# Kernel optimization log

Hardware: AMD Instinct MI355X
Metric: run time of the kernel (lower is better)

The kernel has to match this reference:

```python
import jax, jax.numpy as jnp
import numpy as np

N_NODES = 50000
N_EDGES = 800000
IN_C, HID_C, OUT_C = 128, 128, 64
BN_EPS = 1e-5


def _normalized_adj(edge_index, N):
    # Mirrors remove_self_loops + add_self_loops + symmetric GCN normalization.
    src, dst = edge_index[0], edge_index[1]
    mask = (src != dst).astype(jnp.float32)  # drop original self loops
    # degree of dst over (masked edges + added self loops)
    deg = jax.ops.segment_sum(mask, dst, num_segments=N) + 1.0
    dinv = jnp.where(deg > 0, deg ** -0.5, 0.0)
    w = mask * dinv[src] * dinv[dst]          # weights for original edges
    w_self = dinv * dinv                      # weights for added self loops
    return src, dst, w, w_self


def _spmm(src, dst, w, w_self, x):
    # torch.sparse.mm(adj, x): out[i] = sum_{e: src[e]=i} w[e] * x[dst[e]] + w_self[i]*x[i]
    agg = jax.ops.segment_sum(w[:, None] * x[dst], src, num_segments=x.shape[0])
    return agg + w_self[:, None] * x


def setup_inputs() -> dict:
    key = jax.random.key(0)
    ks = jax.random.split(key, 4)
    x = jax.random.normal(ks[0], (N_NODES, IN_C), dtype=jnp.float32)
    edge_index = jax.random.randint(ks[1], (2, N_EDGES), 0, N_NODES, dtype=jnp.int64)
    # glorot init for GCN linear weights
    s1 = np.sqrt(6.0 / (IN_C + HID_C)).astype(np.float32)
    s2 = np.sqrt(6.0 / (HID_C + OUT_C)).astype(np.float32)
    W1 = jax.random.uniform(ks[2], (IN_C, HID_C), jnp.float32, -s1, s1)
    W2 = jax.random.uniform(ks[3], (HID_C, OUT_C), jnp.float32, -s2, s2)
    return {
        "x": x,
        "edge_index": edge_index,
        "W1": W1,
        "b1": jnp.zeros((HID_C,), jnp.float32),
        "gamma": jnp.ones((HID_C,), jnp.float32),
        "beta": jnp.zeros((HID_C,), jnp.float32),
        "W2": W2,
        "b2": jnp.zeros((OUT_C,), jnp.float32),
    }


def reference(x, edge_index, W1, b1, gamma, beta, W2, b2):
    N = x.shape[0]
    src, dst, w, w_self = _normalized_adj(edge_index, N)
    # layer 1: linear -> SpMM -> BN (batch stats) -> ReLU (dropout: eval)
    h = x @ W1 + b1
    h = _spmm(src, dst, w, w_self, h)
    mean = h.mean(axis=0)
    var = jnp.mean((h - mean) ** 2, axis=0)
    h = (h - mean) * jax.lax.rsqrt(var + BN_EPS) * gamma + beta
    h = jax.nn.relu(h)
    # layer 2: linear -> SpMM
    h = h @ W2 + b2
    h = _spmm(src, dst, w, w_self, h)
    return h
```

## Files before the change

kernel.cpp:

```cpp
#include <hip/hip_runtime.h>

#define N_NODES 50000
#define N_EDGES 800000
#define BN_EPS 1e-5f
#define NPAD 50176
#define SCAN_BLOCKS 98

#define S_SLICES 64
#define R_RANGES 4
#define BINS 16384
#define NP4 (R_RANGES * BINS)
#define ES (N_EDGES / S_SLICES)

#define XS_STRIDE 68

typedef unsigned int uint;
typedef unsigned short ushort;
typedef float floatx4 __attribute__((ext_vector_type(4)));
typedef short bf16x8 __attribute__((ext_vector_type(8)));

__device__ __forceinline__ float bfl(uint u) { return __uint_as_float(u << 16); }
__device__ __forceinline__ float bfh(uint u) { return __uint_as_float(u & 0xffff0000u); }
__device__ __forceinline__ uint pack_bf2(float a, float b) {
    uint ua = __float_as_uint(a), ub = __float_as_uint(b);
    ua += 0x7fffu + ((ua >> 16) & 1u);
    ub += 0x7fffu + ((ub >> 16) & 1u);
    return (ua >> 16) | (ub & 0xffff0000u);
}
__device__ __forceinline__ ushort bf1(float x) {
    uint u = __float_as_uint(x);
    u += 0x7fffu + ((u >> 16) & 1u);
    return (ushort)(u >> 16);
}
__device__ __forceinline__ void acc8(float* a, uint4 h, float w) {
    a[0] += w * bfl(h.x); a[1] += w * bfh(h.x);
    a[2] += w * bfl(h.y); a[3] += w * bfh(h.y);
    a[4] += w * bfl(h.z); a[5] += w * bfh(h.z);
    a[6] += w * bfl(h.w); a[7] += w * bfh(h.w);
}

__global__ __launch_bounds__(256) void prep_w_kernel(const float* __restrict__ W1,
                                                     const float* __restrict__ W2,
                                                     uint* __restrict__ W1t,
                                                     uint* __restrict__ W2t) {
    int t = blockIdx.x * 256 + threadIdx.x;
    if (t < 8192) {
        int n = t >> 6, kk = t & 63;
        W1t[t] = pack_bf2(W1[(2 * kk) * 128 + n], W1[(2 * kk + 1) * 128 + n]);
    } else if (t < 12288) {
        int u = t - 8192;
        int n = u >> 6, kk = u & 63;
        W2t[u] = pack_bf2(W2[(2 * kk) * 64 + n], W2[(2 * kk + 1) * 64 + n]);
    }
}

__global__ __launch_bounds__(256) void count_hist_kernel(const int* __restrict__ src,
                                                         const int* __restrict__ dst,
                                                         ushort* __restrict__ part_cnt,
                                                         ushort* __restrict__ part_deg) {
    __shared__ uint cnt_lds[BINS / 2];
    __shared__ uint deg_lds[BINS / 2];
    const int s = blockIdx.x / R_RANGES;
    const int r = blockIdx.x % R_RANGES;
    const int base = r * BINS;
    for (int j = threadIdx.x; j < BINS / 2; j += 256) { cnt_lds[j] = 0u; deg_lds[j] = 0u; }
    __syncthreads();
    const int4* s4 = (const int4*)(src + s * ES);
    const int4* d4 = (const int4*)(dst + s * ES);
#pragma unroll 2
    for (int g = threadIdx.x; g < ES / 4; g += 256) {
        int4 sv = s4[g];
        int4 dv = d4[g];
#pragma unroll
        for (int k = 0; k < 4; ++k) {
            int ss = (&sv.x)[k], dd = (&dv.x)[k];
            if (ss != dd) {
                int a = ss - base;
                if ((unsigned)a < (unsigned)BINS)
                    atomicAdd(&cnt_lds[a >> 1], 1u << ((a & 1) * 16));
                int b = dd - base;
                if ((unsigned)b < (unsigned)BINS)
                    atomicAdd(&deg_lds[b >> 1], 1u << ((b & 1) * 16));
            }
        }
    }
    __syncthreads();
    uint* pc = (uint*)&part_cnt[s * NP4 + base];
    uint* pd = (uint*)&part_deg[s * NP4 + base];
    for (int j = threadIdx.x; j < BINS / 2; j += 256) { pc[j] = cnt_lds[j]; pd[j] = deg_lds[j]; }
}

__global__ __launch_bounds__(256) void reduce_scan_kernel(const ushort* __restrict__ part_deg,
                                                          const ushort* __restrict__ part_cnt,
                                                          float* __restrict__ dinv,
                                                          int* __restrict__ rowcnt,
                                                          int* __restrict__ rowptr,
                                                          int* __restrict__ psum,
                                                          float* __restrict__ stats) {
    const int t = threadIdx.x;
    if (blockIdx.x == 0) stats[t] = 0.f;
    const int i = blockIdx.x * 512 + 2 * t;
    uint dg0 = 0, dg1 = 0, rc0 = 0, rc1 = 0;
#pragma unroll 8
    for (int s = 0; s < S_SLICES; ++s) {
        uint vd = *(const uint*)&part_deg[s * NP4 + i];
        uint vc = *(const uint*)&part_cnt[s * NP4 + i];
        dg0 += vd & 0xffffu; dg1 += vd >> 16;
        rc0 += vc & 0xffffu; rc1 += vc >> 16;
    }
    *(int2*)&rowcnt[i] = make_int2((int)rc0, (int)rc1);
    if (i < N_NODES) dinv[i] = rsqrtf((float)dg0 + 1.0f);
    if (i + 1 < N_NODES) dinv[i + 1] = rsqrtf((float)dg1 + 1.0f);

    __shared__ int bs[256];
    const int pair = (int)(rc0 + rc1);
    bs[t] = pair;
    __syncthreads();
#pragma unroll
    for (int off = 1; off < 256; off <<= 1) {
        int x = (t >= off) ? bs[t - off] : 0;
        __syncthreads();
        bs[t] += x;
        __syncthreads();
    }
    const int excl = bs[t] - pair;
    *(int2*)&rowptr[i] = make_int2(excl + (int)rc0, excl + pair);
    if (t == 255) psum[blockIdx.x] = bs[255];
}

__global__ __launch_bounds__(256) void cursor_init_kernel(const int* __restrict__ rowcnt,
                                                          int* __restrict__ rowptr,
                                                          const int* __restrict__ psum,
                                                          const ushort* __restrict__ part_cnt,
                                                          int* __restrict__ cursor) {
    __shared__ int pbuf[SCAN_BLOCKS];
    __shared__ int lps;
    const int t = threadIdx.x;
    if (t < SCAN_BLOCKS) pbuf[t] = psum[t];
    __syncthreads();
    if (t == 0) {
        int acc = 0;
        for (int j = 0; j < (int)blockIdx.x; ++j) acc += pbuf[j];
        lps = acc;
    }
    __syncthreads();
    const int ps = lps;
    const int i = blockIdx.x * 512 + 2 * t;
    int b0 = rowptr[i] - rowcnt[i] + ps;
    int b1 = rowptr[i + 1] - rowcnt[i + 1] + ps;
    *(int2*)&rowptr[i] = make_int2(b0, b1);
#pragma unroll 8
    for (int s = 0; s < S_SLICES; ++s) {
        *(int2*)&cursor[s * NP4 + i] = make_int2(b0, b1);
        uint vc = *(const uint*)&part_cnt[s * NP4 + i];
        b0 += (int)(vc & 0xffffu);
        b1 += (int)(vc >> 16);
    }
}

__global__ __launch_bounds__(256) void fill_lds_kernel(const int* __restrict__ src,
                                                       const int* __restrict__ dst,
                                                       const float* __restrict__ dinv,
                                                       const int* __restrict__ cursor,
                                                       int2* __restrict__ epair) {
    __shared__ int curs[BINS];
    const int s = blockIdx.x / R_RANGES;
    const int r = blockIdx.x % R_RANGES;
    const int base = r * BINS;
    const int* gc = &cursor[s * NP4 + base];
    for (int j = threadIdx.x; j < BINS; j += 256) curs[j] = gc[j];
    __syncthreads();
    const int4* s4 = (const int4*)(src + s * ES);
    const int4* d4 = (const int4*)(dst + s * ES);
#pragma unroll 2
    for (int g = threadIdx.x; g < ES / 4; g += 256) {
        int4 sv = s4[g];
        int4 dv = d4[g];
#pragma unroll
        for (int k = 0; k < 4; ++k) {
            int ss = (&sv.x)[k], dd = (&dv.x)[k];
            int a = ss - base;
            if (ss != dd && (unsigned)a < (unsigned)BINS) {
                int pos = atomicAdd(&curs[a], 1);
                epair[pos] = make_int2(dd, __float_as_int(dinv[ss] * dinv[dd]));
            }
        }
    }
}

__global__ __launch_bounds__(256) void gemm1_mfma_kernel(const float* __restrict__ X,
                                                         const uint* __restrict__ W1t,
                                                         const float* __restrict__ bias,
                                                         ushort* __restrict__ Hbf) {
    __shared__ uint lds[(64 + 128) * XS_STRIDE];
    uint* Xs = lds;
    uint* Ws = lds + 64 * XS_STRIDE;
    const int t = threadIdx.x;
    const int rowBase = blockIdx.x * 64;

    {
        int r = t >> 2, q = t & 3;
        int arow = rowBase + r;
        uint* xd = &Xs[r * XS_STRIDE + q * 16];
        if (arow < N_NODES) {
            const float4* xp = (const float4*)&X[arow * 128 + q * 32];
#pragma unroll
            for (int i = 0; i < 8; ++i) {
                float4 v = xp[i];
                xd[2 * i]     = pack_bf2(v.x, v.y);
                xd[2 * i + 1] = pack_bf2(v.z, v.w);
            }
        } else {
#pragma unroll
            for (int i = 0; i < 16; ++i) xd[i] = 0u;
        }
    }
    {
        int n = t >> 1, half = t & 1;
        const uint4* wp = (const uint4*)&W1t[n * 64 + half * 32];
        uint* wd = &Ws[n * XS_STRIDE + half * 32];
#pragma unroll
        for (int i = 0; i < 8; ++i) *(uint4*)&wd[i * 4] = wp[i];
    }
    __syncthreads();

    const int wv = t >> 6, lane = t & 63;
    const int lr = lane & 15;
    const int ko = (lane >> 4) * 4;
    const int m0 = wv * 16;
    floatx4 acc[8];
#pragma unroll
    for (int j = 0; j < 8; ++j) acc[j] = (floatx4){0.f, 0.f, 0.f, 0.f};

#pragma unroll
    for (int ks = 0; ks < 4; ++ks) {
        const int kb = ks * 16 + ko;
        bf16x8 a = *(bf16x8*)&Xs[(m0 + lr) * XS_STRIDE + kb];
#pragma unroll
        for (int j = 0; j < 8; ++j) {
            bf16x8 b = *(bf16x8*)&Ws[(j * 16 + lr) * XS_STRIDE + kb];
            acc[j] = __builtin_amdgcn_mfma_f32_16x16x32_bf16(a, b, acc[j], 0, 0, 0);
        }
    }
    const int rbase = rowBase + m0 + (lane >> 4) * 4;
#pragma unroll
    for (int j = 0; j < 8; ++j) {
        const int col = j * 16 + lr;
        const float bb = bias[col];
#pragma unroll
        for (int r = 0; r < 4; ++r) {
            int row = rbase + r;
            if (row < N_NODES) Hbf[row * 128 + col] = bf1(acc[j][r] + bb);
        }
    }
}

__global__ __launch_bounds__(256) void gemm2_mfma_kernel(const uint* __restrict__ Hin,
                                                         const uint* __restrict__ W2t,
                                                         const float* __restrict__ bias,
                                                         const float* __restrict__ sum,
                                                         const float* __restrict__ sumsq,
                                                         const float* __restrict__ gamma,
                                                         const float* __restrict__ beta,
                                                         ushort* __restrict__ Hbf) {
    __shared__ uint lds[(64 + 64) * XS_STRIDE];
    __shared__ float sc_sh[128], sh_sh[128];
    uint* Xs = lds;
    uint* Ws = lds + 64 * XS_STRIDE;
    const int t = threadIdx.x;
    const int rowBase = blockIdx.x * 64;

    if (t < 128) {
        float mean = sum[t] * (1.0f / N_NODES);
        float var = sumsq[t] * (1.0f / N_NODES) - mean * mean;
        float sc = gamma[t] * rsqrtf(var + BN_EPS);
        sc_sh[t] = sc;
        sh_sh[t] = beta[t] - mean * sc;
    }
    if (t >= 128) {
        int u = t - 128;
        int n = u >> 1, half = u & 1;
        const uint4* wp = (const uint4*)&W2t[n * 64 + half * 32];
        uint* wd = &Ws[n * XS_STRIDE + half * 32];
#pragma unroll
        for (int i = 0; i < 8; ++i) *(uint4*)&wd[i * 4] = wp[i];
    }
    __syncthreads();

    {
        int r = t >> 2, q = t & 3;
        int arow = rowBase + r;
        uint* xd = &Xs[r * XS_STRIDE + q * 16];
        if (arow < N_NODES) {
            const uint* hp = &Hin[arow * 64 + q * 16];
#pragma unroll
            for (int i = 0; i < 16; ++i) {
                uint u = hp[i];
                int m = q * 16 + i;
                float a0 = fmaxf(0.f, bfl(u) * sc_sh[2 * m] + sh_sh[2 * m]);
                float a1 = fmaxf(0.f, bfh(u) * sc_sh[2 * m + 1] + sh_sh[2 * m + 1]);
                xd[i] = pack_bf2(a0, a1);
            }
        } else {
#pragma unroll
            for (int i = 0; i < 16; ++i) xd[i] = 0u;
        }
    }
    __syncthreads();

    const int wv = t >> 6, lane = t & 63;
    const int lr = lane & 15;
    const int ko = (lane >> 4) * 4;
    const int m0 = wv * 16;
    floatx4 acc[4];
#pragma unroll
    for (int j = 0; j < 4; ++j) acc[j] = (floatx4){0.f, 0.f, 0.f, 0.f};

#pragma unroll
    for (int ks = 0; ks < 4; ++ks) {
        const int kb = ks * 16 + ko;
        bf16x8 a = *(bf16x8*)&Xs[(m0 + lr) * XS_STRIDE + kb];
#pragma unroll
        for (int j = 0; j < 4; ++j) {
            bf16x8 b = *(bf16x8*)&Ws[(j * 16 + lr) * XS_STRIDE + kb];
            acc[j] = __builtin_amdgcn_mfma_f32_16x16x32_bf16(a, b, acc[j], 0, 0, 0);
        }
    }
    const int rbase = rowBase + m0 + (lane >> 4) * 4;
#pragma unroll
    for (int j = 0; j < 4; ++j) {
        const int col = j * 16 + lr;
        const float bb = bias[col];
#pragma unroll
        for (int r = 0; r < 4; ++r) {
            int row = rbase + r;
            if (row < N_NODES) Hbf[row * 64 + col] = bf1(acc[j][r] + bb);
        }
    }
}

template <int C, bool OUT_BF16>
__global__ __launch_bounds__(256) void spmm_bf16_kernel(const int* __restrict__ rowptr,
                                                        const int2* __restrict__ epair,
                                                        const float* __restrict__ dinv,
                                                        const uint* __restrict__ H,
                                                        void* __restrict__ outv) {
    constexpr int LPR = C / 8;
    constexpr int RPB = 256 / LPR;
    constexpr int US  = C / 2;
    const int t = threadIdx.x;
    const int lane = t % LPR;
    const int row = blockIdx.x * RPB + t / LPR;
    if (row >= N_NODES) return;
    const int cu = lane * 4;
    const float di = dinv[row];

    float acc[8];
    {
        uint4 hv = *(const uint4*)&H[row * US + cu];
        float w = di * di;
        acc[0] = w * bfl(hv.x); acc[1] = w * bfh(hv.x);
        acc[2] = w * bfl(hv.y); acc[3] = w * bfh(hv.y);
        acc[4] = w * bfl(hv.z); acc[5] = w * bfh(hv.z);
        acc[6] = w * bfl(hv.w); acc[7] = w * bfh(hv.w);
    }
    const int e0 = rowptr[row], e1 = rowptr[row + 1];
    int e = e0;
    if ((e & 1) && e < e1) {
        int2 p = epair[e];
        uint4 h = *(const uint4*)&H[p.x * US + cu];
        acc8(acc, h, __int_as_float(p.y));
        ++e;
    }
    const int4* ep4 = (const int4*)epair;
    for (; e + 8 <= e1; e += 8) {
        int4 qa = ep4[(e >> 1) + 0];
        int4 qb = ep4[(e >> 1) + 1];
        int4 qc = ep4[(e >> 1) + 2];
        int4 qd = ep4[(e >> 1) + 3];
        uint4 h0 = *(const uint4*)&H[qa.x * US + cu];
        uint4 h1 = *(const uint4*)&H[qa.z * US + cu];
        uint4 h2 = *(const uint4*)&H[qb.x * US + cu];
        uint4 h3 = *(const uint4*)&H[qb.z * US + cu];
        uint4 h4 = *(const uint4*)&H[qc.x * US + cu];
        uint4 h5 = *(const uint4*)&H[qc.z * US + cu];
        uint4 h6 = *(const uint4*)&H[qd.x * US + cu];
        uint4 h7 = *(const uint4*)&H[qd.z * US + cu];
        acc8(acc, h0, __int_as_float(qa.y));
        acc8(acc, h1, __int_as_float(qa.w));
        acc8(acc, h2, __int_as_float(qb.y));
        acc8(acc, h3, __int_as_float(qb.w));
        acc8(acc, h4, __int_as_float(qc.y));
        acc8(acc, h5, __int_as_float(qc.w));
        acc8(acc, h6, __int_as_float(qd.y));
        acc8(acc, h7, __int_as_float(qd.w));
    }
    for (; e + 2 <= e1; e += 2) {
        int4 q = ep4[e >> 1];
        uint4 h0 = *(const uint4*)&H[q.x * US + cu];
        uint4 h1 = *(const uint4*)&H[q.z * US + cu];
        acc8(acc, h0, __int_as_float(q.y));
        acc8(acc, h1, __int_as_float(q.w));
    }
    if (e < e1) {
        int2 p = epair[e];
        uint4 h = *(const uint4*)&H[p.x * US + cu];
        acc8(acc, h, __int_as_float(p.y));
    }
    if (OUT_BF16) {
        uint4 o;
        o.x = pack_bf2(acc[0], acc[1]);
        o.y = pack_bf2(acc[2], acc[3]);
        o.z = pack_bf2(acc[4], acc[5]);
        o.w = pack_bf2(acc[6], acc[7]);
        *(uint4*)&((uint*)outv)[row * US + cu] = o;
    } else {
        float* out = (float*)outv;
        *(float4*)&out[row * C + lane * 8]     = make_float4(acc[0], acc[1], acc[2], acc[3]);
        *(float4*)&out[row * C + lane * 8 + 4] = make_float4(acc[4], acc[5], acc[6], acc[7]);
    }
}

__global__ __launch_bounds__(256) void bn_stats_kernel(const uint* __restrict__ H,
                                                       float* __restrict__ sum,
                                                       float* __restrict__ sumsq) {
    int uc = threadIdx.x & 63;
    int quarter = threadIdx.x >> 6;
    float s0 = 0.f, q0 = 0.f, s1 = 0.f, q1 = 0.f;
    for (int r = blockIdx.x * 4 + quarter; r < N_NODES; r += 512) {
        uint u = H[r * 64 + uc];
        float a = bfl(u), b = bfh(u);
        s0 += a; q0 += a * a;
        s1 += b; q1 += b * b;
    }
    __shared__ float red[4][256];
    red[0][threadIdx.x] = s0; red[1][threadIdx.x] = q0;
    red[2][threadIdx.x] = s1; red[3][threadIdx.x] = q1;
    __syncthreads();
    if (quarter == 0) {
        float ts0 = 0.f, tq0 = 0.f, ts1 = 0.f, tq1 = 0.f;
#pragma unroll
        for (int k = 0; k < 4; ++k) {
            ts0 += red[0][k * 64 + uc]; tq0 += red[1][k * 64 + uc];
            ts1 += red[2][k * 64 + uc]; tq1 += red[3][k * 64 + uc];
        }
        atomicAdd(&sum[2 * uc], ts0);
        atomicAdd(&sum[2 * uc + 1], ts1);
        atomicAdd(&sumsq[2 * uc], tq0);
        atomicAdd(&sumsq[2 * uc + 1], tq1);
    }
}

extern "C" void kernel_launch(void* const* d_in, const int* in_sizes, int n_in,
                              void* d_out, int out_size, void* d_ws, size_t ws_size,
                              hipStream_t stream) {
    const float* x     = (const float*)d_in[0];
    const int*   ei    = (const int*)d_in[1];
    const float* W1    = (const float*)d_in[2];
    const float* b1    = (const float*)d_in[3];
    const float* gamma = (const float*)d_in[4];
    const float* beta  = (const float*)d_in[5];
    const float* W2    = (const float*)d_in[6];
    const float* b2    = (const float*)d_in[7];
    float* out = (float*)d_out;
    const int* src = ei;
    const int* dst = ei + N_EDGES;

    float* ws     = (float*)d_ws;
    float* dinv   = ws;
    float* stats  = ws + NPAD;
    int*   psum   = (int*)(ws + NPAD + 512);
    int*   rowcnt = psum + 128;
    int*   rowptr = rowcnt + NPAD;
    float* big    = (float*)(rowptr + NPAD);
    int2*   epair    = (int2*)big;
    ushort* part_cnt = (ushort*)(big + 1600000);
    ushort* part_deg = (ushort*)(big + 3700000);
    int*    cursor   = (int*)(big + 5800000);
    ushort* h1bf     = (ushort*)(big + 1600000);
    uint*   h1agg    = (uint*)(big + 4800000);
    ushort* h2bf     = h1bf;
    uint*   W1t      = (uint*)(big + 10000000);
    uint*   W2t      = W1t + 8192;
    float* sum    = stats;
    float* sumsq  = stats + 128;

    prep_w_kernel<<<48, 256, 0, stream>>>(W1, W2, W1t, W2t);

    count_hist_kernel<<<S_SLICES * R_RANGES, 256, 0, stream>>>(src, dst, part_cnt, part_deg);
    reduce_scan_kernel<<<SCAN_BLOCKS, 256, 0, stream>>>(part_deg, part_cnt, dinv, rowcnt,
                                                        rowptr, psum, stats);
    cursor_init_kernel<<<SCAN_BLOCKS, 256, 0, stream>>>(rowcnt, rowptr, psum, part_cnt, cursor);
    fill_lds_kernel<<<S_SLICES * R_RANGES, 256, 0, stream>>>(src, dst, dinv, cursor, epair);

    gemm1_mfma_kernel<<<(N_NODES + 63) / 64, 256, 0, stream>>>(x, W1t, b1, h1bf);

    spmm_bf16_kernel<128, true><<<(N_NODES + 15) / 16, 256, 0, stream>>>(
        rowptr, epair, dinv, (const uint*)h1bf, (void*)h1agg);

    bn_stats_kernel<<<128, 256, 0, stream>>>(h1agg, sum, sumsq);

    gemm2_mfma_kernel<<<(N_NODES + 63) / 64, 256, 0, stream>>>(h1agg, W2t, b2, sum, sumsq,
                                                               gamma, beta, h2bf);

    spmm_bf16_kernel<64, false><<<(N_NODES + 31) / 32, 256, 0, stream>>>(
        rowptr, epair, dinv, (const uint*)h2bf, (void*)out);
}
```

Measured before the change: 244.9 us.

## Fuse BN statistics into SpMM, merge weight prep into histogram, use byte counters

The batch-norm sum and sum-of-squares are now accumulated inside the first SpMM through LDS atomics, followed by one global atomic per channel per block. This removes the separate bn_stats pass that re-read the aggregated layer-1 output. Weight transposition and packing moves into an extra block of the histogram kernel, saving a launch. Per-slice histogram counters shrink from 16 to 8 bits, halving partial-count traffic, but a node that gets 256 or more edges in one slice would overflow its counter. The statistics are also taken from fp32 accumulators before bf16 rounding rather than from the stored bf16 values.

```diff
diff --git a/kernel.cpp b/kernel.cpp
--- a/kernel.cpp
+++ b/kernel.cpp
@@ -16,6 +16,7 @@
 
 typedef unsigned int uint;
 typedef unsigned short ushort;
+typedef unsigned char uchar;
 typedef float floatx4 __attribute__((ext_vector_type(4)));
 typedef short bf16x8 __attribute__((ext_vector_type(8)));
 
@@ -39,31 +40,33 @@
     a[6] += w * bfl(h.w); a[7] += w * bfh(h.w);
 }
 
-__global__ __launch_bounds__(256) void prep_w_kernel(const float* __restrict__ W1,
-                                                     const float* __restrict__ W2,
-                                                     uint* __restrict__ W1t,
-                                                     uint* __restrict__ W2t) {
-    int t = blockIdx.x * 256 + threadIdx.x;
-    if (t < 8192) {
-        int n = t >> 6, kk = t & 63;
-        W1t[t] = pack_bf2(W1[(2 * kk) * 128 + n], W1[(2 * kk + 1) * 128 + n]);
-    } else if (t < 12288) {
-        int u = t - 8192;
-        int n = u >> 6, kk = u & 63;
-        W2t[u] = pack_bf2(W2[(2 * kk) * 64 + n], W2[(2 * kk + 1) * 64 + n]);
-    }
-}
-
 __global__ __launch_bounds__(256) void count_hist_kernel(const int* __restrict__ src,
                                                          const int* __restrict__ dst,
-                                                         ushort* __restrict__ part_cnt,
-                                                         ushort* __restrict__ part_deg) {
-    __shared__ uint cnt_lds[BINS / 2];
-    __shared__ uint deg_lds[BINS / 2];
+                                                         const float* __restrict__ W1,
+                                                         const float* __restrict__ W2,
+                                                         uint* __restrict__ W1t,
+                                                         uint* __restrict__ W2t,
+                                                         uchar* __restrict__ part_cnt,
+                                                         uchar* __restrict__ part_deg) {
+    if (blockIdx.x == S_SLICES * R_RANGES) {
+        for (int t = threadIdx.x; t < 12288; t += 256) {
+            if (t < 8192) {
+                int n = t >> 6, kk = t & 63;
+                W1t[t] = pack_bf2(W1[(2 * kk) * 128 + n], W1[(2 * kk + 1) * 128 + n]);
+            } else {
+                int u = t - 8192;
+                int n = u >> 6, kk = u & 63;
+                W2t[u] = pack_bf2(W2[(2 * kk) * 64 + n], W2[(2 * kk + 1) * 64 + n]);
+            }
+        }
+        return;
+    }
+    __shared__ uint cnt_lds[BINS / 4];
+    __shared__ uint deg_lds[BINS / 4];
     const int s = blockIdx.x / R_RANGES;
     const int r = blockIdx.x % R_RANGES;
     const int base = r * BINS;
-    for (int j = threadIdx.x; j < BINS / 2; j += 256) { cnt_lds[j] = 0u; deg_lds[j] = 0u; }
+    for (int j = threadIdx.x; j < BINS / 4; j += 256) { cnt_lds[j] = 0u; deg_lds[j] = 0u; }
     __syncthreads();
     const int4* s4 = (const int4*)(src + s * ES);
     const int4* d4 = (const int4*)(dst + s * ES);
@@ -77,21 +80,21 @@
             if (ss != dd) {
                 int a = ss - base;
                 if ((unsigned)a < (unsigned)BINS)
-                    atomicAdd(&cnt_lds[a >> 1], 1u << ((a & 1) * 16));
+                    atomicAdd(&cnt_lds[a >> 2], 1u << ((a & 3) * 8));
                 int b = dd - base;
                 if ((unsigned)b < (unsigned)BINS)
-                    atomicAdd(&deg_lds[b >> 1], 1u << ((b & 1) * 16));
+                    atomicAdd(&deg_lds[b >> 2], 1u << ((b & 3) * 8));
             }
         }
     }
     __syncthreads();
     uint* pc = (uint*)&part_cnt[s * NP4 + base];
     uint* pd = (uint*)&part_deg[s * NP4 + base];
-    for (int j = threadIdx.x; j < BINS / 2; j += 256) { pc[j] = cnt_lds[j]; pd[j] = deg_lds[j]; }
-}
-
-__global__ __launch_bounds__(256) void reduce_scan_kernel(const ushort* __restrict__ part_deg,
-                                                          const ushort* __restrict__ part_cnt,
+    for (int j = threadIdx.x; j < BINS / 4; j += 256) { pc[j] = cnt_lds[j]; pd[j] = deg_lds[j]; }
+}
+
+__global__ __launch_bounds__(256) void reduce_scan_kernel(const uchar* __restrict__ part_deg,
+                                                          const uchar* __restrict__ part_cnt,
                                                           float* __restrict__ dinv,
                                                           int* __restrict__ rowcnt,
                                                           int* __restrict__ rowptr,
@@ -103,10 +106,10 @@
     uint dg0 = 0, dg1 = 0, rc0 = 0, rc1 = 0;
 #pragma unroll 8
     for (int s = 0; s < S_SLICES; ++s) {
-        uint vd = *(const uint*)&part_deg[s * NP4 + i];
-        uint vc = *(const uint*)&part_cnt[s * NP4 + i];
-        dg0 += vd & 0xffffu; dg1 += vd >> 16;
-        rc0 += vc & 0xffffu; rc1 += vc >> 16;
+        uint vd = *(const ushort*)&part_deg[s * NP4 + i];
+        uint vc = *(const ushort*)&part_cnt[s * NP4 + i];
+        dg0 += vd & 0xffu; dg1 += vd >> 8;
+        rc0 += vc & 0xffu; rc1 += vc >> 8;
     }
     *(int2*)&rowcnt[i] = make_int2((int)rc0, (int)rc1);
     if (i < N_NODES) dinv[i] = rsqrtf((float)dg0 + 1.0f);
@@ -131,7 +134,7 @@
 __global__ __launch_bounds__(256) void cursor_init_kernel(const int* __restrict__ rowcnt,
                                                           int* __restrict__ rowptr,
                                                           const int* __restrict__ psum,
-                                                          const ushort* __restrict__ part_cnt,
+                                                          const uchar* __restrict__ part_cnt,
                                                           int* __restrict__ cursor) {
     __shared__ int pbuf[SCAN_BLOCKS];
     __shared__ int lps;
@@ -152,9 +155,9 @@
 #pragma unroll 8
     for (int s = 0; s < S_SLICES; ++s) {
         *(int2*)&cursor[s * NP4 + i] = make_int2(b0, b1);
-        uint vc = *(const uint*)&part_cnt[s * NP4 + i];
-        b0 += (int)(vc & 0xffffu);
-        b1 += (int)(vc >> 16);
+        uint vc = *(const ushort*)&part_cnt[s * NP4 + i];
+        b0 += (int)(vc & 0xffu);
+        b1 += (int)(vc >> 8);
     }
 }
 
@@ -339,19 +342,25 @@
     }
 }
 
-template <int C, bool OUT_BF16>
+template <int C, bool OUT_BF16, bool BN>
 __global__ __launch_bounds__(256) void spmm_bf16_kernel(const int* __restrict__ rowptr,
                                                         const int2* __restrict__ epair,
                                                         const float* __restrict__ dinv,
                                                         const uint* __restrict__ H,
-                                                        void* __restrict__ outv) {
+                                                        void* __restrict__ outv,
+                                                        float* __restrict__ stats) {
     constexpr int LPR = C / 8;
     constexpr int RPB = 256 / LPR;
     constexpr int US  = C / 2;
+    __shared__ float bns[BN ? 256 : 1];
     const int t = threadIdx.x;
+    if (BN) {
+        bns[t] = 0.f;
+        __syncthreads();
+    }
     const int lane = t % LPR;
     const int row = blockIdx.x * RPB + t / LPR;
-    if (row >= N_NODES) return;
+    if (!BN && row >= N_NODES) return;
     const int cu = lane * 4;
     const float di = dinv[row];
 
@@ -419,35 +428,14 @@
         *(float4*)&out[row * C + lane * 8]     = make_float4(acc[0], acc[1], acc[2], acc[3]);
         *(float4*)&out[row * C + lane * 8 + 4] = make_float4(acc[4], acc[5], acc[6], acc[7]);
     }
-}
-
-__global__ __launch_bounds__(256) void bn_stats_kernel(const uint* __restrict__ H,
-                                                       float* __restrict__ sum,
-                                                       float* __restrict__ sumsq) {
-    int uc = threadIdx.x & 63;
-    int quarter = threadIdx.x >> 6;
-    float s0 = 0.f, q0 = 0.f, s1 = 0.f, q1 = 0.f;
-    for (int r = blockIdx.x * 4 + quarter; r < N_NODES; r += 512) {
-        uint u = H[r * 64 + uc];
-        float a = bfl(u), b = bfh(u);
-        s0 += a; q0 += a * a;
-        s1 += b; q1 += b * b;
-    }
-    __shared__ float red[4][256];
-    red[0][threadIdx.x] = s0; red[1][threadIdx.x] = q0;
-    red[2][threadIdx.x] = s1; red[3][threadIdx.x] = q1;
-    __syncthreads();
-    if (quarter == 0) {
-        float ts0 = 0.f, tq0 = 0.f, ts1 = 0.f, tq1 = 0.f;
-#pragma unroll
-        for (int k = 0; k < 4; ++k) {
-            ts0 += red[0][k * 64 + uc]; tq0 += red[1][k * 64 + uc];
-            ts1 += red[2][k * 64 + uc]; tq1 += red[3][k * 64 + uc];
-        }
-        atomicAdd(&sum[2 * uc], ts0);
-        atomicAdd(&sum[2 * uc + 1], ts1);
-        atomicAdd(&sumsq[2 * uc], tq0);
-        atomicAdd(&sumsq[2 * uc + 1], tq1);
+    if (BN) {
+#pragma unroll
+        for (int j = 0; j < 8; ++j) {
+            atomicAdd(&bns[lane * 8 + j], acc[j]);
+            atomicAdd(&bns[128 + lane * 8 + j], acc[j] * acc[j]);
+        }
+        __syncthreads();
+        atomicAdd(&stats[t], bns[t]);
     }
 }
 
@@ -474,8 +462,8 @@
     int*   rowptr = rowcnt + NPAD;
     float* big    = (float*)(rowptr + NPAD);
     int2*   epair    = (int2*)big;
-    ushort* part_cnt = (ushort*)(big + 1600000);
-    ushort* part_deg = (ushort*)(big + 3700000);
+    uchar*  part_cnt = (uchar*)(big + 1600000);
+    uchar*  part_deg = (uchar*)(big + 3700000);
     int*    cursor   = (int*)(big + 5800000);
     ushort* h1bf     = (ushort*)(big + 1600000);
     uint*   h1agg    = (uint*)(big + 4800000);
@@ -485,9 +473,8 @@
     float* sum    = stats;
     float* sumsq  = stats + 128;
 
-    prep_w_kernel<<<48, 256, 0, stream>>>(W1, W2, W1t, W2t);
-
-    count_hist_kernel<<<S_SLICES * R_RANGES, 256, 0, stream>>>(src, dst, part_cnt, part_deg);
+    count_hist_kernel<<<S_SLICES * R_RANGES + 1, 256, 0, stream>>>(src, dst, W1, W2, W1t, W2t,
+                                                                   part_cnt, part_deg);
     reduce_scan_kernel<<<SCAN_BLOCKS, 256, 0, stream>>>(part_deg, part_cnt, dinv, rowcnt,
                                                         rowptr, psum, stats);
     cursor_init_kernel<<<SCAN_BLOCKS, 256, 0, stream>>>(rowcnt, rowptr, psum, part_cnt, cursor);
@@ -495,14 +482,12 @@
 
     gemm1_mfma_kernel<<<(N_NODES + 63) / 64, 256, 0, stream>>>(x, W1t, b1, h1bf);
 
-    spmm_bf16_kernel<128, true><<<(N_NODES + 15) / 16, 256, 0, stream>>>(
-        rowptr, epair, dinv, (const uint*)h1bf, (void*)h1agg);
-
-    bn_stats_kernel<<<128, 256, 0, stream>>>(h1agg, sum, sumsq);
+    spmm_bf16_kernel<128, true, true><<<N_NODES / 16, 256, 0, stream>>>(
+        rowptr, epair, dinv, (const uint*)h1bf, (void*)h1agg, stats);
 
     gemm2_mfma_kernel<<<(N_NODES + 63) / 64, 256, 0, stream>>>(h1agg, W2t, b2, sum, sumsq,
                                                                gamma, beta, h2bf);
 
-    spmm_bf16_kernel<64, false><<<(N_NODES + 31) / 32, 256, 0, stream>>>(
-        rowptr, epair, dinv, (const uint*)h2bf, (void*)out);
-}
+    spmm_bf16_kernel<64, false, false><<<(N_NODES + 31) / 32, 256, 0, stream>>>(
+        rowptr, epair, dinv, (const uint*)h2bf, (void*)out, nullptr);
+}
```

After: 296.0 us. +20.9%, slower.
